# Performance work log

Hardware: AMD Instinct MI355X
Metric: run time of the kernel (lower is better)

Reference implementation:

```python
import jax, jax.numpy as jnp
import numpy as np

F_IN = 10000
M = 3
CARD = 5
LOG_2PI = float(np.log(2.0 * np.pi))


def _normal_logprob(x, means, stds):
    # x: [N, F, 1]; means/stds: [1, F, M] -> [N, F, M]
    z = (x - means) / stds
    return -0.5 * (z * z) - jnp.log(stds) - 0.5 * LOG_2PI


def _sum_layer(x, w):
    # x: [N, F, Cin]; w: [F, Cin, Cout] -> [N, F, Cout]
    logw = jax.nn.log_softmax(w, axis=1)
    return jax.scipy.special.logsumexp(x[:, :, :, None] + logw[None], axis=2)


def _product_layer(x, card):
    # log-domain product = segmented sum over blocks of `card` features
    n, f, c = x.shape
    return x.reshape(n, f // card, card, c).sum(axis=2)


def setup_inputs() -> dict:
    key = jax.random.key(0)
    ks = jax.random.split(key, 9)
    x = jax.random.normal(ks[0], (4096, F_IN), dtype=jnp.float32)
    means = jax.random.normal(ks[1], (1, F_IN, M), dtype=jnp.float32)
    stds = jax.random.uniform(ks[2], (1, F_IN, M), dtype=jnp.float32, minval=0.5, maxval=1.5)
    w1 = jax.random.normal(ks[3], (F_IN, M, 1), dtype=jnp.float32)
    w2 = jax.random.normal(ks[4], (F_IN // 5, 1, 1), dtype=jnp.float32)
    w3 = jax.random.normal(ks[5], (F_IN // 25, 1, 1), dtype=jnp.float32)
    w4 = jax.random.normal(ks[6], (F_IN // 125, 1, 1), dtype=jnp.float32)
    w5 = jax.random.normal(ks[7], (F_IN // 625, 1, 1), dtype=jnp.float32)
    rand_idxs = jax.random.permutation(ks[8], F_IN).astype(jnp.int32)
    return {"x": x, "means": means, "stds": stds, "w1": w1, "w2": w2,
            "w3": w3, "w4": w4, "w5": w5, "rand_idxs": rand_idxs}


def reference(x, means, stds, w1, w2, w3, w4, w5, rand_idxs):
    # scope permutation gather
    xp = x[:, rand_idxs]                          # [N, F]
    y = _normal_logprob(xp[:, :, None], means, stds)  # [N, F, M]
    y = _sum_layer(y, w1)                          # [N, F, 1]
    y = _product_layer(y, CARD)                    # [N, F/5, 1]
    y = _sum_layer(y, w2)
    y = _product_layer(y, CARD)                    # [N, F/25, 1]
    y = _sum_layer(y, w3)
    y = _product_layer(y, CARD)                    # [N, F/125, 1]
    y = _sum_layer(y, w4)
    y = _product_layer(y, CARD)                    # [N, F/625, 1]
    y = _sum_layer(y, w5)
    y = _product_layer(y, F_IN // 5 ** 4)          # [N, 1, 1]
    return y
```

## Files before the change

kernel.cpp:

```cpp
#include <hip/hip_runtime.h>
#include <math.h>

#define F_IN 10000
#define NROWS 4096
#define NCHUNK 40
#define CGROUPS 8
#define ROWS_PER_WAVE 8

__global__ void spn_prep_kernel(const float* __restrict__ means,
                                const float* __restrict__ stds,
                                const float* __restrict__ w1,
                                const int* __restrict__ rand_idxs,
                                float* __restrict__ ws,
                                float* __restrict__ out) {
    int f = blockIdx.x * blockDim.x + threadIdx.x;
    if (f < NROWS) out[f] = 0.0f;
    if (f >= F_IN) return;

    int j = rand_idxs[f];

    float wa = w1[f * 3 + 0];
    float wb = w1[f * 3 + 1];
    float wc = w1[f * 3 + 2];
    float wm = fmaxf(fmaxf(wa, wb), wc);
    float lse = wm + __logf(__expf(wa - wm) + __expf(wb - wm) + __expf(wc - wm));

    const float INV_SQRT2 = 0.70710678118654752440f;
    const float HALF_LOG_2PI = 0.91893853320467274178f;

#pragma unroll
    for (int m = 0; m < 3; m++) {
        float w  = w1[f * 3 + m] - lse;
        float sd = stds[f * 3 + m];
        float mu = means[f * 3 + m];
        float a  = INV_SQRT2 / sd;
        float b  = -mu * a;
        float c  = w - __logf(sd) - HALF_LOG_2PI;
        ws[(0 + m) * F_IN + j] = a;
        ws[(3 + m) * F_IN + j] = b;
        ws[(6 + m) * F_IN + j] = c;
    }
}

__device__ __forceinline__ void col_term(float xv,
                                         float a0, float b0, float c0,
                                         float a1, float b1, float c1,
                                         float a2, float b2, float c2,
                                         float& mx_out, float& s_out) {
    float u0 = fmaf(xv, a0, b0);
    float u1 = fmaf(xv, a1, b1);
    float u2 = fmaf(xv, a2, b2);
    float v0 = fmaf(-u0, u0, c0);
    float v1 = fmaf(-u1, u1, c1);
    float v2 = fmaf(-u2, u2, c2);
    float mx = fmaxf(fmaxf(v0, v1), v2);
    float me = __builtin_amdgcn_fmed3f(v0, v1, v2);
    float mn = fminf(fminf(v0, v1), v2);
    float s  = 1.0f + __expf(me - mx) + __expf(mn - mx);
    mx_out = mx;
    s_out  = s;
}

__global__ __launch_bounds__(256) void spn_main_kernel(const float* __restrict__ x,
                                                       const float* __restrict__ ws,
                                                       float* __restrict__ out) {
    const int wave = threadIdx.x >> 6;
    const int lane = threadIdx.x & 63;
    const int rb   = blockIdx.x >> 3;
    const int cg   = blockIdx.x & 7;
    const int row0 = rb * 32 + wave * ROWS_PER_WAVE;

    float accm[ROWS_PER_WAVE];
    float prod[ROWS_PER_WAVE];
#pragma unroll
    for (int r = 0; r < ROWS_PER_WAVE; r++) { accm[r] = 0.0f; prod[r] = 1.0f; }

    for (int c = cg; c < NCHUNK; c += CGROUPS) {
        int j4 = c * 256 + lane * 4;
        bool valid = (j4 < F_IN);
        int jc = valid ? j4 : 0;
        int q  = jc >> 2;

        const float4 A0 = ((const float4*)(ws + 0 * F_IN))[q];
        const float4 A1 = ((const float4*)(ws + 1 * F_IN))[q];
        const float4 A2 = ((const float4*)(ws + 2 * F_IN))[q];
        const float4 B0 = ((const float4*)(ws + 3 * F_IN))[q];
        const float4 B1 = ((const float4*)(ws + 4 * F_IN))[q];
        const float4 B2 = ((const float4*)(ws + 5 * F_IN))[q];
        const float4 C0 = ((const float4*)(ws + 6 * F_IN))[q];
        const float4 C1 = ((const float4*)(ws + 7 * F_IN))[q];
        const float4 C2 = ((const float4*)(ws + 8 * F_IN))[q];

#pragma unroll
        for (int r = 0; r < ROWS_PER_WAVE; r++) {
            const float4 xv = *(const float4*)(x + (row0 + r) * F_IN + jc);

            float m0, s0, m1, s1, m2, s2, m3, s3;
            col_term(xv.x, A0.x, B0.x, C0.x, A1.x, B1.x, C1.x, A2.x, B2.x, C2.x, m0, s0);
            col_term(xv.y, A0.y, B0.y, C0.y, A1.y, B1.y, C1.y, A2.y, B2.y, C2.y, m1, s1);
            col_term(xv.z, A0.z, B0.z, C0.z, A1.z, B1.z, C1.z, A2.z, B2.z, C2.z, m2, s2);
            col_term(xv.w, A0.w, B0.w, C0.w, A1.w, B1.w, C1.w, A2.w, B2.w, C2.w, m3, s3);

            float smx = (m0 + m1) + (m2 + m3);
            float sp  = (s0 * s1) * (s2 * s3);
            accm[r] += valid ? smx : 0.0f;
            prod[r] *= valid ? sp : 1.0f;
        }
    }

#pragma unroll
    for (int r = 0; r < ROWS_PER_WAVE; r++) {
        float part = accm[r] + __logf(prod[r]);
#pragma unroll
        for (int off = 32; off > 0; off >>= 1)
            part += __shfl_xor(part, off, 64);
        if (lane == 0)
            atomicAdd(&out[row0 + r], part);
    }
}

extern "C" void kernel_launch(void* const* d_in, const int* in_sizes, int n_in,
                              void* d_out, int out_size, void* d_ws, size_t ws_size,
                              hipStream_t stream) {
    const float* x         = (const float*)d_in[0];
    const float* means     = (const float*)d_in[1];
    const float* stds      = (const float*)d_in[2];
    const float* w1        = (const float*)d_in[3];
    const int*   rand_idxs = (const int*)d_in[8];

    float* out = (float*)d_out;
    float* ws  = (float*)d_ws;

    spn_prep_kernel<<<(F_IN + 255) / 256, 256, 0, stream>>>(means, stds, w1, rand_idxs, ws, out);

    spn_main_kernel<<<128 * CGROUPS, 256, 0, stream>>>(x, ws, out);
}
```

Measured before the change: 249.8 us.

## Software-prefetch x rows across chunk iterations and halve rows per wave

The chunk loop is now fully unrolled over its 5 iterations and loads the next chunk's x values into registers before computing the current chunk, so global load latency overlaps with the math. Rows per wave drop from 8 to 4 and the grid doubles to 2048 blocks, which gives more waves for latency hiding. The cost is more blocks, each reloading the ws coefficient vectors, more atomics on the output, and extra registers for the double-buffered x values.

```diff
diff --git a/kernel.cpp b/kernel.cpp
--- a/kernel.cpp
+++ b/kernel.cpp
@@ -5,7 +5,7 @@
 #define NROWS 4096
 #define NCHUNK 40
 #define CGROUPS 8
-#define ROWS_PER_WAVE 8
+#define ROWS_PER_WAVE 4
 
 __global__ void spn_prep_kernel(const float* __restrict__ means,
                                 const float* __restrict__ stds,
@@ -68,18 +68,31 @@
     const int lane = threadIdx.x & 63;
     const int rb   = blockIdx.x >> 3;
     const int cg   = blockIdx.x & 7;
-    const int row0 = rb * 32 + wave * ROWS_PER_WAVE;
+    const int row0 = rb * (ROWS_PER_WAVE * 4) + wave * ROWS_PER_WAVE;
 
     float accm[ROWS_PER_WAVE];
     float prod[ROWS_PER_WAVE];
 #pragma unroll
     for (int r = 0; r < ROWS_PER_WAVE; r++) { accm[r] = 0.0f; prod[r] = 1.0f; }
 
-    for (int c = cg; c < NCHUNK; c += CGROUPS) {
-        int j4 = c * 256 + lane * 4;
-        bool valid = (j4 < F_IN);
-        int jc = valid ? j4 : 0;
-        int q  = jc >> 2;
+    const float* xr[ROWS_PER_WAVE];
+#pragma unroll
+    for (int r = 0; r < ROWS_PER_WAVE; r++) xr[r] = x + (size_t)(row0 + r) * F_IN;
+
+    float4 xv[ROWS_PER_WAVE];
+    {
+        int jc = cg * 256 + lane * 4;
+#pragma unroll
+        for (int r = 0; r < ROWS_PER_WAVE; r++)
+            xv[r] = *(const float4*)(xr[r] + jc);
+    }
+
+#pragma unroll
+    for (int it = 0; it < 5; ++it) {
+        const int c = cg + it * 8;
+        const int jcur = c * 256 + lane * 4;
+        const bool vcur = (jcur < F_IN);
+        const int q = vcur ? (jcur >> 2) : 0;
 
         const float4 A0 = ((const float4*)(ws + 0 * F_IN))[q];
         const float4 A1 = ((const float4*)(ws + 1 * F_IN))[q];
@@ -91,20 +104,32 @@
         const float4 C1 = ((const float4*)(ws + 7 * F_IN))[q];
         const float4 C2 = ((const float4*)(ws + 8 * F_IN))[q];
 
+        float4 xn[ROWS_PER_WAVE];
+        if (it < 4) {
+            int jn = (c + 8) * 256 + lane * 4;
+            int jnc = (jn < F_IN) ? jn : 0;
+#pragma unroll
+            for (int r = 0; r < ROWS_PER_WAVE; r++)
+                xn[r] = *(const float4*)(xr[r] + jnc);
+        }
+
 #pragma unroll
         for (int r = 0; r < ROWS_PER_WAVE; r++) {
-            const float4 xv = *(const float4*)(x + (row0 + r) * F_IN + jc);
-
             float m0, s0, m1, s1, m2, s2, m3, s3;
-            col_term(xv.x, A0.x, B0.x, C0.x, A1.x, B1.x, C1.x, A2.x, B2.x, C2.x, m0, s0);
-            col_term(xv.y, A0.y, B0.y, C0.y, A1.y, B1.y, C1.y, A2.y, B2.y, C2.y, m1, s1);
-            col_term(xv.z, A0.z, B0.z, C0.z, A1.z, B1.z, C1.z, A2.z, B2.z, C2.z, m2, s2);
-            col_term(xv.w, A0.w, B0.w, C0.w, A1.w, B1.w, C1.w, A2.w, B2.w, C2.w, m3, s3);
+            col_term(xv[r].x, A0.x, B0.x, C0.x, A1.x, B1.x, C1.x, A2.x, B2.x, C2.x, m0, s0);
+            col_term(xv[r].y, A0.y, B0.y, C0.y, A1.y, B1.y, C1.y, A2.y, B2.y, C2.y, m1, s1);
+            col_term(xv[r].z, A0.z, B0.z, C0.z, A1.z, B1.z, C1.z, A2.z, B2.z, C2.z, m2, s2);
+            col_term(xv[r].w, A0.w, B0.w, C0.w, A1.w, B1.w, C1.w, A2.w, B2.w, C2.w, m3, s3);
 
             float smx = (m0 + m1) + (m2 + m3);
             float sp  = (s0 * s1) * (s2 * s3);
-            accm[r] += valid ? smx : 0.0f;
-            prod[r] *= valid ? sp : 1.0f;
+            accm[r] += vcur ? smx : 0.0f;
+            prod[r] *= vcur ? sp : 1.0f;
+        }
+
+        if (it < 4) {
+#pragma unroll
+            for (int r = 0; r < ROWS_PER_WAVE; r++) xv[r] = xn[r];
         }
     }
 
@@ -133,5 +158,5 @@
 
     spn_prep_kernel<<<(F_IN + 255) / 256, 256, 0, stream>>>(means, stds, w1, rand_idxs, ws, out);
 
-    spn_main_kernel<<<128 * CGROUPS, 256, 0, stream>>>(x, ws, out);
+    spn_main_kernel<<<256 * CGROUPS, 256, 0, stream>>>(x, ws, out);
 }
```

Result: no change. 247.4 us, median of 2 (-0.9%).
